# Kernel tuning notes

Measured on AMD Instinct MI355X. Metric: run time of the kernel, lower is better.

## Reference

```python
import jax, jax.numpy as jnp
import numpy as np

K = 3          # kernel size
SH, SW = 2, 1  # stride
PH, PW = 1, 1  # padding


def conv2d(x, w, b, stride, pad):
    y = jax.lax.conv_general_dilated(
        x, w, window_strides=stride,
        padding=[(pad[0], pad[0]), (pad[1], pad[1])],
        dimension_numbers=('NCHW', 'OIHW', 'NCHW'))
    return y + b[None, :, None, None]


def setup_inputs() -> dict:
    key = jax.random.key(0)
    ks = jax.random.split(key, 4)
    x = jax.random.normal(ks[0], (8, 64, 128, 128), jnp.float32)
    # scale offset weights small so sampled offsets are O(1) pixels (exercises
    # the bilinear path without sampling far out of bounds)
    w_offset = jax.random.normal(ks[1], (18, 64, 3, 3), jnp.float32) * 0.02
    b_offset = jnp.zeros((18,), jnp.float32)
    w_mask = jax.random.normal(ks[2], (9, 64, 3, 3), jnp.float32) * 0.05
    b_mask = jnp.zeros((9,), jnp.float32)
    w_conv = jax.random.normal(ks[3], (64, 64, 3, 3), jnp.float32) * (1.0 / 24.0)
    return dict(x=x, w_offset=w_offset, b_offset=b_offset,
                w_mask=w_mask, b_mask=b_mask, w_conv=w_conv)


def _bilinear_gather(x, py, px):
    # x: [B,C,H,W]; py, px: [B,K2,Ho,Wo] float sampling coordinates.
    # Zero-padding outside the image (torchvision deform_conv2d semantics).
    B, C, H, W = x.shape
    y0f = jnp.floor(py)
    x0f = jnp.floor(px)
    dy = py - y0f
    dx = px - x0f
    y0 = y0f.astype(jnp.int32)
    x0 = x0f.astype(jnp.int32)

    def corner(yi, xi, wgt):
        valid = (yi >= 0) & (yi < H) & (xi >= 0) & (xi < W)
        yc = jnp.clip(yi, 0, H - 1)
        xc = jnp.clip(xi, 0, W - 1)
        # per-batch fancy gather -> [B, C, K2, Ho, Wo]
        g = jax.vmap(lambda xb, yb, xbi: xb[:, yb, xbi])(x, yc, xc)
        return g * (wgt * valid)[:, None]

    return (corner(y0,     x0,     (1 - dy) * (1 - dx))
            + corner(y0,     x0 + 1, (1 - dy) * dx)
            + corner(y0 + 1, x0,     dy * (1 - dx))
            + corner(y0 + 1, x0 + 1, dy * dx))


def reference(x, w_offset, b_offset, w_mask, b_mask, w_conv):
    B, C, H, W = x.shape
    offset = conv2d(x, w_offset, b_offset, (SH, SW), (PH, PW))   # [B, 2*K2, Ho, Wo]
    mask = jax.nn.sigmoid(conv2d(x, w_mask, b_mask, (SH, SW), (PH, PW)))  # [B, K2, Ho, Wo]
    Ho, Wo = offset.shape[2], offset.shape[3]
    K2 = K * K
    off = offset.reshape(B, K2, 2, Ho, Wo)
    off_y = off[:, :, 0]   # [B,K2,Ho,Wo]
    off_x = off[:, :, 1]
    ky = (jnp.arange(K2) // K).astype(jnp.float32)
    kx = (jnp.arange(K2) % K).astype(jnp.float32)
    hs = (jnp.arange(Ho) * SH - PH).astype(jnp.float32)
    ws = (jnp.arange(Wo) * SW - PW).astype(jnp.float32)
    py = off_y + ky[None, :, None, None] + hs[None, None, :, None]
    px = off_x + kx[None, :, None, None] + ws[None, None, None, :]
    sampled = _bilinear_gather(x, py, px) * mask[:, None]  # [B,C,K2,Ho,Wo]
    # weighted accumulate over in-channels and kernel taps
    out = jnp.einsum('ock,bckhw->bohw', w_conv.reshape(-1, C, K2), sampled)
    return out
```

## Files before the change

kernel.cpp:

```cpp
#include <hip/hip_runtime.h>
#include <hip/hip_bf16.h>
#include <hip/hip_fp16.h>
#include <math.h>

#define BB 8
#define CC 64
#define HH 128
#define WW 128
#define HO 64
#define WO 128
#define OC 64
#define HW (HH * WW)
#define HOWO (HO * WO)

typedef __attribute__((ext_vector_type(8))) short short8;
typedef __attribute__((ext_vector_type(4))) float floatx4;

union BfBits { __hip_bfloat16 h; unsigned short s; };
__device__ __forceinline__ unsigned short f2bf(float f) {
    BfBits b; b.h = __float2bfloat16(f); return b.s;
}
__device__ __forceinline__ float bflo(unsigned int u) {
    return __uint_as_float(u << 16);
}
__device__ __forceinline__ float bfhi(unsigned int u) {
    return __uint_as_float(u & 0xFFFF0000u);
}

__global__ __launch_bounds__(256) void prep(
    const float* __restrict__ x,
    const float* __restrict__ w_off, const float* __restrict__ w_msk,
    const float* __restrict__ w_conv,
    unsigned short* __restrict__ xT, unsigned int* __restrict__ xP,
    unsigned short* __restrict__ Wom, unsigned short* __restrict__ W2)
{
    __shared__ float T[64][130];
    int tid = threadIdx.x;
    int bx = blockIdx.x;
    if (bx < 1024) {
        int b = bx & 7, y = bx >> 3;
        int wl = tid & 127, c0 = tid >> 7;
#pragma unroll
        for (int i = 0; i < 32; ++i) {
            int c = 2 * i + c0;
            T[c][wl] = x[(((size_t)b * CC + c) * HH + y) * WW + wl];
        }
        __syncthreads();
        int c = tid & 63, wg = tid >> 6;
#pragma unroll
        for (int i = 0; i < 32; ++i) {
            int wp = wg * 32 + i;
            unsigned int lo = f2bf(T[c][wp]);
            unsigned int hi = (wp < 127) ? f2bf(T[c][wp + 1]) : 0u;
            size_t e = (((size_t)b * HH + y) * WW + wp) * 64 + c;
            xT[e] = (unsigned short)lo;
            xP[e] = lo | (hi << 16);
        }
    } else if (bx < 1096) {
        int i = (bx - 1024) * 256 + tid;
        int ch = i / 576, kk = i % 576;
        int xs = kk >> 6, c = kk & 63;
        float v = 0.0f;
        if (ch < 18)      v = w_off[(ch * CC + c) * 9 + xs];
        else if (ch < 27) v = w_msk[((ch - 18) * CC + c) * 9 + xs];
        Wom[i] = f2bf(v);
    } else {
        int i = (bx - 1096) * 256 + tid;
        int k = i % 9, c = (i / 9) % CC, o = i / (CC * 9);
        W2[((size_t)k * OC + o) * CC + c] = f2bf(w_conv[i]);
    }
}

__global__ __launch_bounds__(256) void fused(
    const unsigned short* __restrict__ xT, const unsigned int* __restrict__ xP,
    const unsigned short* __restrict__ Wom, const unsigned short* __restrict__ W2,
    const float* __restrict__ b_off, const float* __restrict__ b_msk,
    float* __restrict__ out)
{
    __shared__ __align__(16) char lds[18304];
    typedef unsigned short XsRow[34][72];
    XsRow* Xs = (XsRow*)lds;
    unsigned short (*S)[32][64] = (unsigned short(*)[32][64])lds;
    uint4* meta = (uint4*)(lds + 8192);
    float (*omr)[33] = (float(*)[33])(lds + 14720);

    int tid = threadIdx.x;
    int lane = tid & 63;
    int wv = __builtin_amdgcn_readfirstlane(tid >> 6);
    int bx = blockIdx.x;
    int b = bx & 7;
    int rest = bx >> 3;
    int h = rest >> 2;
    int w0 = (rest & 3) * 32;
    int h2 = 2 * h - 1;
    int m16 = lane & 15, q = lane >> 4;

    for (int u = tid; u < 816; u += 256) {
        int ky = u / 272;
        int rem = u - ky * 272;
        int col = rem >> 3, cb = rem & 7;
        int hy = h2 + ky, wc = w0 - 1 + col;
        short8 v = {0, 0, 0, 0, 0, 0, 0, 0};
        if ((unsigned)hy < (unsigned)HH && (unsigned)wc < (unsigned)WW)
            v = *(const short8*)(xT + (((size_t)b * HH + hy) * WW + wc) * 64 + cb * 8);
        *(short8*)&Xs[ky][col][cb * 8] = v;
    }
    __syncthreads();

    {
        int mt = wv & 1, nt = wv >> 1;
        floatx4 a = (floatx4){0.f, 0.f, 0.f, 0.f};
        const unsigned short* wa = Wom + (mt * 16 + m16) * 576 + q * 8;
#pragma unroll
        for (int t = 0; t < 18; ++t) {
            int xs = t >> 1, ky = xs / 3, kx = xs % 3;
            short8 af = *(const short8*)(wa + t * 32);
            short8 bf = *(const short8*)&Xs[ky][nt * 16 + m16 + kx][(t & 1) * 32 + q * 8];
            a = __builtin_amdgcn_mfma_f32_16x16x32_bf16(af, bf, a, 0, 0, 0);
        }
#pragma unroll
        for (int r = 0; r < 4; ++r) {
            int ch = mt * 16 + q * 4 + r;
            if (ch < 27) omr[ch][nt * 16 + m16] = a[r];
        }
    }
    __syncthreads();

    for (int u = tid; u < 288; u += 256) {
        int kk = u >> 5, pos = u & 31;
        float offy = omr[2 * kk][pos] + b_off[2 * kk];
        float offx = omr[2 * kk + 1][pos] + b_off[2 * kk + 1];
        float mk = 1.0f / (1.0f + __expf(-(omr[18 + kk][pos] + b_msk[kk])));
        float py = offy + (float)(kk / 3) + (float)h2;
        float px = offx + (float)(kk % 3) + (float)(w0 + pos - 1);

        float y0f = floorf(py), x0f = floorf(px);
        float dy = py - y0f, dx = px - x0f;
        int y0 = (int)y0f, x0 = (int)x0f;
        int y1 = y0 + 1, x1 = x0 + 1;
        bool vy0 = (unsigned)y0 < (unsigned)HH;
        bool vy1 = (unsigned)y1 < (unsigned)HH;
        bool vx0 = (unsigned)x0 < (unsigned)WW;
        bool vx1 = (unsigned)x1 < (unsigned)WW;
        float w00 = (1.0f - dy) * (1.0f - dx) * ((vy0 && vx0) ? mk : 0.0f);
        float w01 = (1.0f - dy) * dx          * ((vy0 && vx1) ? mk : 0.0f);
        float w10 = dy * (1.0f - dx)          * ((vy1 && vx0) ? mk : 0.0f);
        float w11 = dy * dx                   * ((vy1 && vx1) ? mk : 0.0f);
        int xbase = min(max(x0, 0), WW - 2);
        bool s0 = x0 > xbase;
        bool s1 = x1 > xbase;
        float cxA = (s0 ? 0.f : w00) + (s1 ? 0.f : w01);
        float cyA = (s0 ? w00 : 0.f) + (s1 ? w01 : 0.f);
        float cxB = (s0 ? 0.f : w10) + (s1 ? 0.f : w11);
        float cyB = (s0 ? w10 : 0.f) + (s1 ? w11 : 0.f);
        int yc0 = min(max(y0, 0), HH - 1);
        int yc1 = min(max(y1, 0), HH - 1);

        __half2 hA = __floats2half2_rn(cxA, cyA);
        __half2 hB = __floats2half2_rn(cxB, cyB);
        uint4 mu;
        mu.x = __builtin_bit_cast(unsigned int, hA);
        mu.y = __builtin_bit_cast(unsigned int, hB);
        mu.z = (unsigned)(yc0 * WW + xbase) * 256u;
        mu.w = (unsigned)(yc1 * WW + xbase) * 256u;
        meta[u] = mu;
    }
    __syncthreads();

    int p0 = wv * 8;
    int c = lane;
    const char* xPb = (const char*)(xP + (size_t)b * HW * 64);
    floatx4 acc0 = (floatx4){0.f, 0.f, 0.f, 0.f};
    floatx4 acc1 = (floatx4){0.f, 0.f, 0.f, 0.f};

    uint4 M[8];
    unsigned int G0[8], G1[8];

    auto issue = [&](int k) {
#pragma unroll
        for (int i = 0; i < 8; ++i) {
            M[i] = meta[k * 32 + p0 + i];
            G0[i] = *(const unsigned int*)(xPb + M[i].z + 4 * c);
            G1[i] = *(const unsigned int*)(xPb + M[i].w + 4 * c);
        }
    };
    auto store = [&](int buf) {
#pragma unroll
        for (int i = 0; i < 8; ++i) {
            __half2 hA = __builtin_bit_cast(__half2, M[i].x);
            __half2 hB = __builtin_bit_cast(__half2, M[i].y);
            float v = __low2float(hA) * bflo(G0[i]) + __high2float(hA) * bfhi(G0[i])
                    + __low2float(hB) * bflo(G1[i]) + __high2float(hB) * bfhi(G1[i]);
            int pos = p0 + i;
            S[buf][pos][((c >> 3) ^ (pos & 7)) * 8 + (c & 7)] = f2bf(v);
        }
    };

    issue(0);
    store(0);

#pragma unroll
    for (int k = 0; k < 9; ++k) {
        __syncthreads();
        if (k < 8) issue(k + 1);
        {
            const unsigned short* wk = W2 + ((size_t)(k * OC) + wv * 16 + m16) * CC + q * 8;
            int buf = k & 1;
#pragma unroll
            for (int s = 0; s < 2; ++s) {
                short8 af = *(const short8*)(wk + s * 32);
                int cb = ((q + 4 * s) ^ (m16 & 7)) * 8;
                short8 bf0 = *(const short8*)&S[buf][m16][cb];
                short8 bf1 = *(const short8*)&S[buf][16 + m16][cb];
                acc0 = __builtin_amdgcn_mfma_f32_16x16x32_bf16(af, bf0, acc0, 0, 0, 0);
                acc1 = __builtin_amdgcn_mfma_f32_16x16x32_bf16(af, bf1, acc1, 0, 0, 0);
            }
        }
        if (k < 8) store((k + 1) & 1);
    }

#pragma unroll
    for (int nt = 0; nt < 2; ++nt) {
        floatx4 av = nt ? acc1 : acc0;
#pragma unroll
        for (int r = 0; r < 4; ++r) {
            int o = wv * 16 + q * 4 + r;
            out[(((size_t)b * OC + o) * HO + h) * WO + w0 + nt * 16 + m16] = av[r];
        }
    }
}

extern "C" void kernel_launch(void* const* d_in, const int* in_sizes, int n_in,
                              void* d_out, int out_size, void* d_ws, size_t ws_size,
                              hipStream_t stream)
{
    const float* x      = (const float*)d_in[0];
    const float* w_off  = (const float*)d_in[1];
    const float* b_off  = (const float*)d_in[2];
    const float* w_msk  = (const float*)d_in[3];
    const float* b_msk  = (const float*)d_in[4];
    const float* w_conv = (const float*)d_in[5];
    float* out = (float*)d_out;

    unsigned short* xT = (unsigned short*)d_ws;
    unsigned int* xP = (unsigned int*)(xT + (size_t)BB * HW * 64);
    unsigned short* Wom = (unsigned short*)(xP + (size_t)BB * HW * 64);
    unsigned short* W2 = Wom + 32 * 576;

    prep<<<dim3(1240), dim3(256), 0, stream>>>(x, w_off, w_msk, w_conv,
                                               xT, xP, Wom, W2);
    fused<<<dim3(2048), dim3(256), 0, stream>>>(xT, xP, Wom, W2,
                                                b_off, b_msk, out);
}
```

Measured before the change: 144.5 us.

## Stage all nine tap tiles in LDS and drop per-tap barriers; widen prep blocks

The fused kernel now gathers and writes all nine sampled tap tiles into a larger LDS region before a single barrier, then runs the MFMA loop over all taps with no further barriers. Previously it double-buffered one tap at a time with a barrier per tap. Bilinear coefficients are kept as fp32 float4 instead of packed half2, and the gather row offsets are split into a separate array read through readfirstlane as scalars. The prep kernel moves to 512-thread blocks with a narrower transpose pad. The trade-off is much higher LDS use per block (about 47KB), which may lower occupancy, and the gather and MFMA phases no longer overlap.

```diff
diff --git a/kernel.cpp b/kernel.cpp
--- a/kernel.cpp
+++ b/kernel.cpp
@@ -1,6 +1,5 @@
 #include <hip/hip_runtime.h>
 #include <hip/hip_bf16.h>
-#include <hip/hip_fp16.h>
 #include <math.h>
 
 #define BB 8
@@ -27,37 +26,37 @@
     return __uint_as_float(u & 0xFFFF0000u);
 }
 
-__global__ __launch_bounds__(256) void prep(
+__global__ __launch_bounds__(512) void prep(
     const float* __restrict__ x,
     const float* __restrict__ w_off, const float* __restrict__ w_msk,
     const float* __restrict__ w_conv,
     unsigned short* __restrict__ xT, unsigned int* __restrict__ xP,
     unsigned short* __restrict__ Wom, unsigned short* __restrict__ W2)
 {
-    __shared__ float T[64][130];
+    __shared__ float T[64][129];
     int tid = threadIdx.x;
     int bx = blockIdx.x;
     if (bx < 1024) {
         int b = bx & 7, y = bx >> 3;
         int wl = tid & 127, c0 = tid >> 7;
 #pragma unroll
-        for (int i = 0; i < 32; ++i) {
-            int c = 2 * i + c0;
+        for (int i = 0; i < 16; ++i) {
+            int c = 4 * i + c0;
             T[c][wl] = x[(((size_t)b * CC + c) * HH + y) * WW + wl];
         }
         __syncthreads();
         int c = tid & 63, wg = tid >> 6;
 #pragma unroll
-        for (int i = 0; i < 32; ++i) {
-            int wp = wg * 32 + i;
+        for (int i = 0; i < 16; ++i) {
+            int wp = wg * 16 + i;
             unsigned int lo = f2bf(T[c][wp]);
             unsigned int hi = (wp < 127) ? f2bf(T[c][wp + 1]) : 0u;
             size_t e = (((size_t)b * HH + y) * WW + wp) * 64 + c;
             xT[e] = (unsigned short)lo;
             xP[e] = lo | (hi << 16);
         }
-    } else if (bx < 1096) {
-        int i = (bx - 1024) * 256 + tid;
+    } else if (bx < 1060) {
+        int i = (bx - 1024) * 512 + tid;
         int ch = i / 576, kk = i % 576;
         int xs = kk >> 6, c = kk & 63;
         float v = 0.0f;
@@ -65,7 +64,7 @@
         else if (ch < 27) v = w_msk[((ch - 18) * CC + c) * 9 + xs];
         Wom[i] = f2bf(v);
     } else {
-        int i = (bx - 1096) * 256 + tid;
+        int i = (bx - 1060) * 512 + tid;
         int k = i % 9, c = (i / 9) % CC, o = i / (CC * 9);
         W2[((size_t)k * OC + o) * CC + c] = f2bf(w_conv[i]);
     }
@@ -77,12 +76,13 @@
     const float* __restrict__ b_off, const float* __restrict__ b_msk,
     float* __restrict__ out)
 {
-    __shared__ __align__(16) char lds[18304];
+    __shared__ __align__(16) char lds[47360];
+    unsigned short (*S)[32][64] = (unsigned short(*)[32][64])lds;
     typedef unsigned short XsRow[34][72];
     XsRow* Xs = (XsRow*)lds;
-    unsigned short (*S)[32][64] = (unsigned short(*)[32][64])lds;
-    uint4* meta = (uint4*)(lds + 8192);
-    float (*omr)[33] = (float(*)[33])(lds + 14720);
+    float (*omr)[33] = (float(*)[33])(lds + 36864);
+    uint2*  metaR = (uint2*)(lds + 40432);
+    float4* metaC = (float4*)(lds + 42736);
 
     int tid = threadIdx.x;
     int lane = tid & 63;
@@ -149,74 +149,70 @@
         int xbase = min(max(x0, 0), WW - 2);
         bool s0 = x0 > xbase;
         bool s1 = x1 > xbase;
-        float cxA = (s0 ? 0.f : w00) + (s1 ? 0.f : w01);
-        float cyA = (s0 ? w00 : 0.f) + (s1 ? w01 : 0.f);
-        float cxB = (s0 ? 0.f : w10) + (s1 ? 0.f : w11);
-        float cyB = (s0 ? w10 : 0.f) + (s1 ? w11 : 0.f);
+        float4 cf;
+        cf.x = (s0 ? 0.f : w00) + (s1 ? 0.f : w01);
+        cf.y = (s0 ? w00 : 0.f) + (s1 ? w01 : 0.f);
+        cf.z = (s0 ? 0.f : w10) + (s1 ? 0.f : w11);
+        cf.w = (s0 ? w10 : 0.f) + (s1 ? w11 : 0.f);
         int yc0 = min(max(y0, 0), HH - 1);
         int yc1 = min(max(y1, 0), HH - 1);
-
-        __half2 hA = __floats2half2_rn(cxA, cyA);
-        __half2 hB = __floats2half2_rn(cxB, cyB);
-        uint4 mu;
-        mu.x = __builtin_bit_cast(unsigned int, hA);
-        mu.y = __builtin_bit_cast(unsigned int, hB);
-        mu.z = (unsigned)(yc0 * WW + xbase) * 256u;
-        mu.w = (unsigned)(yc1 * WW + xbase) * 256u;
-        meta[u] = mu;
+        metaC[u] = cf;
+        uint2 mr;
+        mr.x = (unsigned)(yc0 * WW + xbase) * 256u;
+        mr.y = (unsigned)(yc1 * WW + xbase) * 256u;
+        metaR[u] = mr;
     }
     __syncthreads();
 
     int p0 = wv * 8;
     int c = lane;
+    int c4 = 4 * c;
     const char* xPb = (const char*)(xP + (size_t)b * HW * 64);
+    unsigned int G0[2][8], G1[2][8];
+
+    auto issue = [&](int k, int sel) {
+#pragma unroll
+        for (int i = 0; i < 8; ++i) {
+            uint2 mr = metaR[k * 32 + p0 + i];
+            unsigned r0 = __builtin_amdgcn_readfirstlane(mr.x);
+            unsigned r1 = __builtin_amdgcn_readfirstlane(mr.y);
+            G0[sel][i] = *(const unsigned int*)(xPb + r0 + c4);
+            G1[sel][i] = *(const unsigned int*)(xPb + r1 + c4);
+        }
+    };
+    auto store = [&](int k, int sel) {
+#pragma unroll
+        for (int i = 0; i < 8; ++i) {
+            float4 cf = metaC[k * 32 + p0 + i];
+            float v = cf.x * bflo(G0[sel][i]) + cf.y * bfhi(G0[sel][i])
+                    + cf.z * bflo(G1[sel][i]) + cf.w * bfhi(G1[sel][i]);
+            int pos = p0 + i;
+            S[k][pos][((c >> 3) ^ (pos & 7)) * 8 + (c & 7)] = f2bf(v);
+        }
+    };
+
+    issue(0, 0);
+#pragma unroll
+    for (int k = 0; k < 9; ++k) {
+        if (k < 8) issue(k + 1, (k + 1) & 1);
+        store(k, k & 1);
+    }
+    __syncthreads();
+
     floatx4 acc0 = (floatx4){0.f, 0.f, 0.f, 0.f};
     floatx4 acc1 = (floatx4){0.f, 0.f, 0.f, 0.f};
-
-    uint4 M[8];
-    unsigned int G0[8], G1[8];
-
-    auto issue = [&](int k) {
-#pragma unroll
-        for (int i = 0; i < 8; ++i) {
-            M[i] = meta[k * 32 + p0 + i];
-            G0[i] = *(const unsigned int*)(xPb + M[i].z + 4 * c);
-            G1[i] = *(const unsigned int*)(xPb + M[i].w + 4 * c);
-        }
-    };
-    auto store = [&](int buf) {
-#pragma unroll
-        for (int i = 0; i < 8; ++i) {
-            __half2 hA = __builtin_bit_cast(__half2, M[i].x);
-            __half2 hB = __builtin_bit_cast(__half2, M[i].y);
-            float v = __low2float(hA) * bflo(G0[i]) + __high2float(hA) * bfhi(G0[i])
-                    + __low2float(hB) * bflo(G1[i]) + __high2float(hB) * bfhi(G1[i]);
-            int pos = p0 + i;
-            S[buf][pos][((c >> 3) ^ (pos & 7)) * 8 + (c & 7)] = f2bf(v);
-        }
-    };
-
-    issue(0);
-    store(0);
-
 #pragma unroll
     for (int k = 0; k < 9; ++k) {
-        __syncthreads();
-        if (k < 8) issue(k + 1);
-        {
-            const unsigned short* wk = W2 + ((size_t)(k * OC) + wv * 16 + m16) * CC + q * 8;
-            int buf = k & 1;
-#pragma unroll
-            for (int s = 0; s < 2; ++s) {
-                short8 af = *(const short8*)(wk + s * 32);
-                int cb = ((q + 4 * s) ^ (m16 & 7)) * 8;
-                short8 bf0 = *(const short8*)&S[buf][m16][cb];
-                short8 bf1 = *(const short8*)&S[buf][16 + m16][cb];
-                acc0 = __builtin_amdgcn_mfma_f32_16x16x32_bf16(af, bf0, acc0, 0, 0, 0);
-                acc1 = __builtin_amdgcn_mfma_f32_16x16x32_bf16(af, bf1, acc1, 0, 0, 0);
-            }
-        }
-        if (k < 8) store((k + 1) & 1);
+        const unsigned short* wk = W2 + ((size_t)(k * OC) + wv * 16 + m16) * CC + q * 8;
+#pragma unroll
+        for (int s = 0; s < 2; ++s) {
+            short8 af = *(const short8*)(wk + s * 32);
+            int cb = ((q + 4 * s) ^ (m16 & 7)) * 8;
+            short8 bf0 = *(const short8*)&S[k][m16][cb];
+            short8 bf1 = *(const short8*)&S[k][16 + m16][cb];
+            acc0 = __builtin_amdgcn_mfma_f32_16x16x32_bf16(af, bf0, acc0, 0, 0, 0);
+            acc1 = __builtin_amdgcn_mfma_f32_16x16x32_bf16(af, bf1, acc1, 0, 0, 0);
+        }
     }
 
 #pragma unroll
@@ -247,7 +243,7 @@
     unsigned short* Wom = (unsigned short*)(xP + (size_t)BB * HW * 64);
     unsigned short* W2 = Wom + 32 * 576;
 
-    prep<<<dim3(1240), dim3(256), 0, stream>>>(x, w_off, w_msk, w_conv,
+    prep<<<dim3(1132), dim3(512), 0, stream>>>(x, w_off, w_msk, w_conv,
                                                xT, xP, Wom, W2);
     fused<<<dim3(2048), dim3(256), 0, stream>>>(xT, xP, Wom, W2,
                                                 b_off, b_msk, out);
```

Measured after the change: 145.5 us. Within noise of the previous version (+0.7%).
